# Optimization experiments

Hardware: AMD Instinct MI355X
Metric: run time of the kernel (lower is better)

Reference implementation:

```python
import jax, jax.numpy as jnp
import numpy as np

N = 100_000   # nodes
E = 1_600_000 # edges
F = 64        # in_feats
H = 64        # hid
EPS = 1e-5


def setup_inputs() -> dict:
    key = jax.random.key(0)
    ks = jax.random.split(key, 12)
    s = 1.0 / np.sqrt(F)
    inp = {
        "x":   jax.random.normal(ks[0], (N, F), jnp.float32),
        "src": jax.random.randint(ks[1], (E,), 0, N, jnp.int32),
        "dst": jax.random.randint(ks[2], (E,), 0, N, jnp.int32),
        # GraphConv 1: in_feats -> hid
        "W1": jax.random.uniform(ks[3], (F, H), jnp.float32, -s, s),
        "b1": jnp.zeros((H,), jnp.float32),
        "g1": jnp.ones((H,), jnp.float32),
        "be1": jnp.zeros((H,), jnp.float32),
        # GraphConv 2: hid -> hid
        "W2": jax.random.uniform(ks[4], (H, H), jnp.float32, -s, s),
        "b2": jnp.zeros((H,), jnp.float32),
        "g2": jnp.ones((H,), jnp.float32),
        "be2": jnp.zeros((H,), jnp.float32),
        # classifier hid -> 2
        "Wc": jax.random.uniform(ks[5], (H, 2), jnp.float32, -s, s),
        "bc": jnp.zeros((2,), jnp.float32),
    }
    return inp


def _graph_conv(x, src, dst, W, b):
    # DGL GraphConv, norm='both', allow_zero_in_degree=True:
    # h = D_in^{-1/2} A (D_out^{-1/2} x) W + b, degrees clamped to >= 1.
    n = x.shape[0]
    ones = jnp.ones(src.shape[0], x.dtype)
    deg_out = jnp.clip(jax.ops.segment_sum(ones, src, num_segments=n), 1.0)
    deg_in = jnp.clip(jax.ops.segment_sum(ones, dst, num_segments=n), 1.0)
    h = x * jax.lax.rsqrt(deg_out)[:, None]
    m = jax.ops.segment_sum(h[src], dst, num_segments=n)  # gather-scatter SpMM
    m = m * jax.lax.rsqrt(deg_in)[:, None]
    return m @ W + b


def _bn(h, g, be):
    # BatchNorm1d training-mode math over nodes (biased variance).
    mu = h.mean(axis=0)
    var = h.var(axis=0)
    return (h - mu) * jax.lax.rsqrt(var + EPS) * g + be


def reference(x, src, dst, W1, b1, g1, be1, W2, b2, g2, be2, Wc, bc):
    h = jax.nn.relu(_bn(_graph_conv(x, src, dst, W1, b1), g1, be1))
    # dropout is identity in eval mode
    h = jax.nn.relu(_bn(_graph_conv(h, src, dst, W2, b2), g2, be2))
    hg = h.mean(axis=0, keepdims=True)  # [1, H] graph readout
    return hg @ Wc + bc                 # [1, 2]
```

## Files before the change

kernel.cpp:

```cpp
#include <hip/hip_runtime.h>
#include <hip/hip_fp16.h>

#define FDIM 64
#define EPS 1e-5f
#define NBUCK 1024
#define LOWB 7
#define LOWMASK 127
#define RB 256
#define RT 1024
#define GRP 16
#define NSLOT 8

__global__ void k_hist(const int* __restrict__ src, const int* __restrict__ dst,
                       int* __restrict__ histS, int* __restrict__ histD, int E, int chunk) {
    __shared__ int hs[NBUCK], hd[NBUCK];
    int tid = threadIdx.x;
    hs[tid] = 0; hd[tid] = 0;
    __syncthreads();
    int b = blockIdx.x;
    int beg = b * chunk;
    int end = min(E, beg + chunk);
    int i = beg + tid * 4;
    for (; i + 3 < end; i += RT * 4) {
        int4 s = *(const int4*)(src + i);
        int4 d = *(const int4*)(dst + i);
        atomicAdd(&hs[s.x >> LOWB], 1); atomicAdd(&hd[d.x >> LOWB], 1);
        atomicAdd(&hs[s.y >> LOWB], 1); atomicAdd(&hd[d.y >> LOWB], 1);
        atomicAdd(&hs[s.z >> LOWB], 1); atomicAdd(&hd[d.z >> LOWB], 1);
        atomicAdd(&hs[s.w >> LOWB], 1); atomicAdd(&hd[d.w >> LOWB], 1);
    }
    if (i < end) {
        for (int j = i; j < end && j < i + 4; ++j) {
            atomicAdd(&hs[src[j] >> LOWB], 1);
            atomicAdd(&hd[dst[j] >> LOWB], 1);
        }
    }
    __syncthreads();
    histS[b * NBUCK + tid] = hs[tid];
    histD[b * NBUCK + tid] = hd[tid];
}

__global__ void k_scanA(const int* __restrict__ histS, const int* __restrict__ histD,
                        int* __restrict__ psumS, int* __restrict__ psumD) {
    int bid = blockIdx.x;
    int m = bid >> 6;
    int g = (bid >> 2) & (RB / GRP - 1);
    int c = bid & 3;
    const int* hist = m ? histD : histS;
    int* psum = m ? psumD : psumS;
    int k = c * 256 + threadIdx.x;
    int s = 0;
#pragma unroll
    for (int r = 0; r < GRP; ++r)
        s += hist[(g * GRP + r) * NBUCK + k];
    psum[g * NBUCK + k] = s;
}

__global__ void k_scanB(const int* __restrict__ psumS, int* __restrict__ baseS,
                        int* __restrict__ grpbaseS,
                        const int* __restrict__ psumD, int* __restrict__ baseD,
                        int* __restrict__ grpbaseD) {
    const int* psum = blockIdx.x ? psumD : psumS;
    int* base    = blockIdx.x ? baseD : baseS;
    int* grpbase = blockIdx.x ? grpbaseD : grpbaseS;
    __shared__ int s[NBUCK];
    int k = threadIdx.x;
    int ge[RB / GRP];
    int run = 0;
#pragma unroll
    for (int g = 0; g < RB / GRP; ++g) { ge[g] = run; run += psum[g * NBUCK + k]; }
    s[k] = run;
    __syncthreads();
    for (int off = 1; off < NBUCK; off <<= 1) {
        int t = (k >= off) ? s[k - off] : 0;
        __syncthreads();
        s[k] += t;
        __syncthreads();
    }
    int excl = (k > 0) ? s[k - 1] : 0;
    base[k] = excl;
    if (k == NBUCK - 1) base[NBUCK] = s[NBUCK - 1];
#pragma unroll
    for (int g = 0; g < RB / GRP; ++g)
        grpbase[g * NBUCK + k] = excl + ge[g];
}

__global__ void k_bucket(const int* __restrict__ src, const int* __restrict__ dst,
                         const int* __restrict__ histS, const int* __restrict__ histD,
                         const int* __restrict__ grpbaseS, const int* __restrict__ grpbaseD,
                         unsigned char* __restrict__ tmpS, int* __restrict__ tmpD,
                         int E, int chunk) {
    __shared__ int curS[NBUCK], curD[NBUCK];
    int tid = threadIdx.x;
    int b = blockIdx.x;
    int g = b / GRP;
    int rs = 0, rd = 0;
    for (int r = g * GRP; r < b; ++r) {
        rs += histS[r * NBUCK + tid];
        rd += histD[r * NBUCK + tid];
    }
    curS[tid] = grpbaseS[g * NBUCK + tid] + rs;
    curD[tid] = grpbaseD[g * NBUCK + tid] + rd;
    __syncthreads();
    int beg = b * chunk;
    int end = min(E, beg + chunk);
    int i = beg + tid * 4;
    for (; i + 3 < end; i += RT * 4) {
        int4 s = *(const int4*)(src + i);
        int4 d = *(const int4*)(dst + i);
        int p;
        p = atomicAdd(&curS[s.x >> LOWB], 1); tmpS[p] = (unsigned char)(s.x & LOWMASK);
        p = atomicAdd(&curS[s.y >> LOWB], 1); tmpS[p] = (unsigned char)(s.y & LOWMASK);
        p = atomicAdd(&curS[s.z >> LOWB], 1); tmpS[p] = (unsigned char)(s.z & LOWMASK);
        p = atomicAdd(&curS[s.w >> LOWB], 1); tmpS[p] = (unsigned char)(s.w & LOWMASK);
        p = atomicAdd(&curD[d.x >> LOWB], 1); tmpD[p] = (s.x << LOWB) | (d.x & LOWMASK);
        p = atomicAdd(&curD[d.y >> LOWB], 1); tmpD[p] = (s.y << LOWB) | (d.y & LOWMASK);
        p = atomicAdd(&curD[d.z >> LOWB], 1); tmpD[p] = (s.z << LOWB) | (d.z & LOWMASK);
        p = atomicAdd(&curD[d.w >> LOWB], 1); tmpD[p] = (s.w << LOWB) | (d.w & LOWMASK);
    }
    if (i < end) {
        for (int j = i; j < end && j < i + 4; ++j) {
            int sv = src[j], dv = dst[j];
            int p = atomicAdd(&curS[sv >> LOWB], 1);
            tmpS[p] = (unsigned char)(sv & LOWMASK);
            p = atomicAdd(&curD[dv >> LOWB], 1);
            tmpD[p] = (sv << LOWB) | (dv & LOWMASK);
        }
    }
}

__global__ void k_fine(const int* __restrict__ tmpD, const int* __restrict__ baseD,
                       int* __restrict__ csr_src, int* __restrict__ rowptr,
                       const unsigned char* __restrict__ tmpS, const int* __restrict__ baseS,
                       int* __restrict__ degO, const float* __restrict__ x,
                       __half* __restrict__ bufA, int N, int nbuck) {
    __shared__ int hist[128];
    __shared__ int scanv[128];
    int tid = threadIdx.x;
    if (blockIdx.x < nbuck) {
        int b = blockIdx.x;
        int s0 = baseD[b];
        int s1 = baseD[b + 1];
        if (tid < 128) hist[tid] = 0;
        __syncthreads();
        for (int i = s0 + tid; i < s1; i += 256)
            atomicAdd(&hist[tmpD[i] & LOWMASK], 1);
        __syncthreads();
        int mine = (tid < 128) ? hist[tid] : 0;
        if (tid < 128) scanv[tid] = mine;
        __syncthreads();
        for (int off = 1; off < 128; off <<= 1) {
            int t = (tid < 128 && tid >= off) ? scanv[tid - off] : 0;
            __syncthreads();
            if (tid < 128) scanv[tid] += t;
            __syncthreads();
        }
        if (tid < 128) {
            int excl = scanv[tid] - mine;
            int d = (b << LOWB) + tid;
            if (d <= N) rowptr[d] = s0 + excl;
            hist[tid] = excl;
        }
        __syncthreads();
        for (int i = s0 + tid; i < s1; i += 256) {
            int p = tmpD[i];
            int pos = atomicAdd(&hist[p & LOWMASK], 1);
            csr_src[s0 + pos] = p >> LOWB;
        }
    } else {
        int b = blockIdx.x - nbuck;
        int s0 = baseS[b];
        int s1 = baseS[b + 1];
        if (tid < 128) hist[tid] = 0;
        __syncthreads();
        for (int i = s0 + tid; i < s1; i += 256)
            atomicAdd(&hist[tmpS[i]], 1);
        __syncthreads();
        if (tid < 128) {
            int d = (b << LOWB) + tid;
            if (d < N) degO[d] = hist[tid];
        }
        int node = (b << LOWB) + (tid >> 1);
        if (node < N) {
            float rs = rsqrtf((float)max(hist[tid >> 1], 1));
            int part = tid & 1;
            const float4* xr = (const float4*)(x + (size_t)node * FDIM) + part * 8;
            float4* orow = (float4*)(bufA + (size_t)node * FDIM) + part * 4;
#pragma unroll
            for (int q = 0; q < 4; ++q) {
                float4 a = xr[2 * q];
                float4 c = xr[2 * q + 1];
                union { __half2 h[4]; float4 f; } u;
                u.h[0] = __floats2half2_rn(a.x * rs, a.y * rs);
                u.h[1] = __floats2half2_rn(a.z * rs, a.w * rs);
                u.h[2] = __floats2half2_rn(c.x * rs, c.y * rs);
                u.h[3] = __floats2half2_rn(c.z * rs, c.w * rs);
                orow[q] = u.f;
            }
        }
    }
}

__global__ void k_spmm8(const __half* __restrict__ hin, const int* __restrict__ rowptr,
                        const int* __restrict__ csr_src, __half* __restrict__ out, int N) {
    int wid = (blockIdx.x * blockDim.x + threadIdx.x) >> 6;
    int lane = threadIdx.x & 63;
    int g = lane >> 3;
    int sl = lane & 7;
    int row = wid * 8 + g;
    bool rv = row < N;
    int start = rv ? rowptr[row] : 0;
    int end   = rv ? rowptr[row + 1] : 0;
    int deg = end - start;
    int md = deg;
    md = max(md, __shfl_xor(md, 8));
    md = max(md, __shfl_xor(md, 16));
    md = max(md, __shfl_xor(md, 32));
    float acc[8] = {0.f, 0.f, 0.f, 0.f, 0.f, 0.f, 0.f, 0.f};
    for (int it = 0; it < md; it += 8) {
        int a = start + it + sl;
        int ca = (a < end) ? a : ((deg > 0) ? end - 1 : 0);
        int idxv = csr_src[ca];
#pragma unroll
        for (int j = 0; j < 8; ++j) {
            int bidx = __shfl(idxv, (g << 3) + j);
            if (it + j < deg) {
                const float4* gp = (const float4*)(hin + ((size_t)bidx << 6));
                union { float4 f; __half2 h[4]; } u;
                u.f = gp[sl];
                float2 p0 = __half22float2(u.h[0]);
                float2 p1 = __half22float2(u.h[1]);
                float2 p2 = __half22float2(u.h[2]);
                float2 p3 = __half22float2(u.h[3]);
                acc[0] += p0.x; acc[1] += p0.y;
                acc[2] += p1.x; acc[3] += p1.y;
                acc[4] += p2.x; acc[5] += p2.y;
                acc[6] += p3.x; acc[7] += p3.y;
            }
        }
    }
    if (rv) {
        float rs = rsqrtf(fmaxf((float)deg, 1.0f));
        union { float4 f; __half2 h[4]; } o;
        o.h[0] = __floats2half2_rn(acc[0] * rs, acc[1] * rs);
        o.h[1] = __floats2half2_rn(acc[2] * rs, acc[3] * rs);
        o.h[2] = __floats2half2_rn(acc[4] * rs, acc[5] * rs);
        o.h[3] = __floats2half2_rn(acc[6] * rs, acc[7] * rs);
        ((float4*)(out + ((size_t)row << 6)))[sl] = o.f;
    }
}

__global__ void k_gemm_reg(const __half* __restrict__ m, const float* __restrict__ W,
                           const float* __restrict__ b, __half* __restrict__ out, int N) {
    int n = blockIdx.x * blockDim.x + threadIdx.x;
    if (n >= N) return;
    const __half2* mrow = (const __half2*)(m + (size_t)n * FDIM);
    float acc[FDIM];
#pragma unroll
    for (int j = 0; j < FDIM; ++j) acc[j] = b[j];
    for (int k0 = 0; k0 < FDIM; k0 += 8) {
        float2 f0 = __half22float2(mrow[(k0 >> 1) + 0]);
        float2 f1 = __half22float2(mrow[(k0 >> 1) + 1]);
        float2 f2 = __half22float2(mrow[(k0 >> 1) + 2]);
        float2 f3 = __half22float2(mrow[(k0 >> 1) + 3]);
        float mreg[8] = {f0.x, f0.y, f1.x, f1.y, f2.x, f2.y, f3.x, f3.y};
#pragma unroll
        for (int k1 = 0; k1 < 8; ++k1) {
            const float* Wrow = W + (k0 + k1) * FDIM;
#pragma unroll
            for (int j = 0; j < FDIM; ++j)
                acc[j] = fmaf(mreg[k1], Wrow[j], acc[j]);
        }
    }
    float4* orow = (float4*)(out + (size_t)n * FDIM);
#pragma unroll
    for (int j = 0; j < FDIM; j += 8) {
        union { __half2 h[4]; float4 f; } u;
        u.h[0] = __floats2half2_rn(acc[j + 0], acc[j + 1]);
        u.h[1] = __floats2half2_rn(acc[j + 2], acc[j + 3]);
        u.h[2] = __floats2half2_rn(acc[j + 4], acc[j + 5]);
        u.h[3] = __floats2half2_rn(acc[j + 6], acc[j + 7]);
        orow[j >> 3] = u.f;
    }
}

__global__ void k_stats_fin(const __half* __restrict__ h, float* __restrict__ ssum,
                            float* __restrict__ ssq, const float* __restrict__ g,
                            float* __restrict__ mu, float* __restrict__ coef,
                            int* __restrict__ cnt, int N) {
    __shared__ float red[4][128];
    __shared__ int lastv;
    int tid = threadIdx.x;
    int sl = tid & 7;
    int nl = tid >> 3;
    float s[8] = {0.f,0.f,0.f,0.f,0.f,0.f,0.f,0.f};
    float q[8] = {0.f,0.f,0.f,0.f,0.f,0.f,0.f,0.f};
    int stride = gridDim.x * 32;
    for (int n = blockIdx.x * 32 + nl; n < N; n += stride) {
        union { float4 f; __half2 hh[4]; } u;
        u.f = ((const float4*)(h + ((size_t)n << 6)))[sl];
#pragma unroll
        for (int p = 0; p < 4; ++p) {
            float2 v = __half22float2(u.hh[p]);
            s[2*p]   += v.x; q[2*p]   += v.x * v.x;
            s[2*p+1] += v.y; q[2*p+1] += v.y * v.y;
        }
    }
#pragma unroll
    for (int off = 8; off < 64; off <<= 1) {
#pragma unroll
        for (int p = 0; p < 8; ++p) {
            s[p] += __shfl_xor(s[p], off);
            q[p] += __shfl_xor(q[p], off);
        }
    }
    int wv = tid >> 6, lane = tid & 63;
    if (lane < 8) {
#pragma unroll
        for (int p = 0; p < 8; ++p) {
            red[wv][lane * 8 + p] = s[p];
            red[wv][64 + lane * 8 + p] = q[p];
        }
    }
    __syncthreads();
    int slot = (blockIdx.x & (NSLOT - 1)) << 6;
    if (tid < 128) {
        float v = red[0][tid] + red[1][tid] + red[2][tid] + red[3][tid];
        if (tid < 64) atomicAdd(&ssum[slot + tid], v);
        else          atomicAdd(&ssq[slot + tid - 64], v);
    }
    __syncthreads();
    if (tid == 0)
        lastv = (__hip_atomic_fetch_add(cnt, 1, __ATOMIC_ACQ_REL,
                                        __HIP_MEMORY_SCOPE_AGENT) == (int)gridDim.x - 1);
    __syncthreads();
    if (lastv && tid < 64) {
        float sv = 0.f, qv = 0.f;
#pragma unroll
        for (int p = 0; p < NSLOT; ++p) {
            sv += __hip_atomic_load(&ssum[(p << 6) + tid], __ATOMIC_RELAXED,
                                    __HIP_MEMORY_SCOPE_AGENT);
            qv += __hip_atomic_load(&ssq[(p << 6) + tid], __ATOMIC_RELAXED,
                                    __HIP_MEMORY_SCOPE_AGENT);
        }
        float m = sv / (float)N;
        float var = qv / (float)N - m * m;
        mu[tid] = m;
        coef[tid] = rsqrtf(var + EPS) * g[tid];
    }
}

__global__ void k_bnrelu_scale(const float2* __restrict__ h, const float* __restrict__ mu,
                               const float* __restrict__ coef, const float* __restrict__ be,
                               const int* __restrict__ degO, float2* __restrict__ out, int n4) {
    int i = blockIdx.x * blockDim.x + threadIdx.x;
    if (i < n4) {
        int n = i >> 4;
        int j4 = (i & 15) << 2;
        float rs = rsqrtf((float)max(degO[n], 1));
        union { __half2 hh[2]; float2 f; } u;
        u.f = h[i];
        float2 v0 = __half22float2(u.hh[0]);
        float2 v1 = __half22float2(u.hh[1]);
        float r0 = fmaxf((v0.x - mu[j4 + 0]) * coef[j4 + 0] + be[j4 + 0], 0.f) * rs;
        float r1 = fmaxf((v0.y - mu[j4 + 1]) * coef[j4 + 1] + be[j4 + 1], 0.f) * rs;
        float r2 = fmaxf((v1.x - mu[j4 + 2]) * coef[j4 + 2] + be[j4 + 2], 0.f) * rs;
        float r3 = fmaxf((v1.y - mu[j4 + 3]) * coef[j4 + 3] + be[j4 + 3], 0.f) * rs;
        union { __half2 hh[2]; float2 f; } o;
        o.hh[0] = __floats2half2_rn(r0, r1);
        o.hh[1] = __floats2half2_rn(r2, r3);
        out[i] = o.f;
    }
}

__global__ void k_bnmean_fin(const __half* __restrict__ h, const float* __restrict__ mu,
                             const float* __restrict__ coef, const float* __restrict__ be,
                             float* __restrict__ hsum, const float* __restrict__ Wc,
                             const float* __restrict__ bc, float* __restrict__ out,
                             int* __restrict__ cnt, int N) {
    __shared__ float red[4][64];
    __shared__ float cls[128];
    __shared__ int lastv;
    int tid = threadIdx.x;
    int sl = tid & 7;
    int nl = tid >> 3;
    int j8 = sl * 8;
    float m_[8], c_[8], b_[8];
#pragma unroll
    for (int p = 0; p < 8; ++p) { m_[p] = mu[j8 + p]; c_[p] = coef[j8 + p]; b_[p] = be[j8 + p]; }
    float s[8] = {0.f,0.f,0.f,0.f,0.f,0.f,0.f,0.f};
    int stride = gridDim.x * 32;
    for (int n = blockIdx.x * 32 + nl; n < N; n += stride) {
        union { float4 f; __half2 hh[4]; } u;
        u.f = ((const float4*)(h + ((size_t)n << 6)))[sl];
#pragma unroll
        for (int p = 0; p < 4; ++p) {
            float2 v = __half22float2(u.hh[p]);
            s[2*p]   += fmaxf((v.x - m_[2*p])   * c_[2*p]   + b_[2*p],   0.f);
            s[2*p+1] += fmaxf((v.y - m_[2*p+1]) * c_[2*p+1] + b_[2*p+1], 0.f);
        }
    }
#pragma unroll
    for (int off = 8; off < 64; off <<= 1) {
#pragma unroll
        for (int p = 0; p < 8; ++p) s[p] += __shfl_xor(s[p], off);
    }
    int wv = tid >> 6, lane = tid & 63;
    if (lane < 8) {
#pragma unroll
        for (int p = 0; p < 8; ++p) red[wv][lane * 8 + p] = s[p];
    }
    __syncthreads();
    int slot = (blockIdx.x & (NSLOT - 1)) << 6;
    if (tid < 64)
        atomicAdd(&hsum[slot + tid], red[0][tid] + red[1][tid] + red[2][tid] + red[3][tid]);
    __syncthreads();
    if (tid == 0)
        lastv = (__hip_atomic_fetch_add(cnt, 1, __ATOMIC_ACQ_REL,
                                        __HIP_MEMORY_SCOPE_AGENT) == (int)gridDim.x - 1);
    __syncthreads();
    if (lastv) {
        if (tid < 64) {
            float hg = 0.f;
#pragma unroll
            for (int p = 0; p < NSLOT; ++p)
                hg += __hip_atomic_load(&hsum[(p << 6) + tid], __ATOMIC_RELAXED,
                                        __HIP_MEMORY_SCOPE_AGENT);
            hg /= (float)N;
            cls[tid]      = hg * Wc[tid * 2 + 0];
            cls[64 + tid] = hg * Wc[tid * 2 + 1];
        }
        __syncthreads();
        if (tid == 0) {
            float a = 0.f, bv = 0.f;
            for (int k = 0; k < 64; ++k) { a += cls[k]; bv += cls[64 + k]; }
            out[0] = a + bc[0];
            out[1] = bv + bc[1];
        }
    }
}

extern "C" void kernel_launch(void* const* d_in, const int* in_sizes, int n_in,
                              void* d_out, int out_size, void* d_ws, size_t ws_size,
                              hipStream_t stream) {
    const float* x   = (const float*)d_in[0];
    const int*   src = (const int*)d_in[1];
    const int*   dst = (const int*)d_in[2];
    const float* W1  = (const float*)d_in[3];
    const float* b1  = (const float*)d_in[4];
    const float* g1  = (const float*)d_in[5];
    const float* be1 = (const float*)d_in[6];
    const float* W2  = (const float*)d_in[7];
    const float* b2  = (const float*)d_in[8];
    const float* g2  = (const float*)d_in[9];
    const float* be2 = (const float*)d_in[10];
    const float* Wc  = (const float*)d_in[11];
    const float* bc  = (const float*)d_in[12];
    float* out = (float*)d_out;

    const int N = in_sizes[0] / FDIM;
    const int E = in_sizes[1];

    char* w = (char*)d_ws;
    __half* bufA   = (__half*)w;
    __half* bufB   = bufA + (size_t)N * FDIM;
    int*   csr_src = (int*)(bufB + (size_t)N * FDIM);
    int*   degO    = csr_src + E;
    int*   rowptr  = degO + N;
    int*   histS   = rowptr + N + 2;
    int*   histD   = histS + RB * NBUCK;
    int*   baseS   = histD + RB * NBUCK;
    int*   baseD   = baseS + NBUCK + 1;
    int*   psumS   = baseD + NBUCK + 1;
    int*   psumD   = psumS + (RB / GRP) * NBUCK;
    int*   grpbaseS= psumD + (RB / GRP) * NBUCK;
    int*   grpbaseD= grpbaseS + (RB / GRP) * NBUCK;
    float* stats   = (float*)(grpbaseD + (RB / GRP) * NBUCK);
    unsigned char* tmpS = (unsigned char*)(stats + 4096);
    int*           tmpD = (int*)bufB;

    float* sum1  = stats + 0;
    float* sq1   = stats + 512;
    float* sum2  = stats + 1024;
    float* sq2   = stats + 1536;
    float* hsum  = stats + 2048;
    float* mu1   = stats + 2560;
    float* coef1 = stats + 2624;
    float* mu2   = stats + 2688;
    float* coef2 = stats + 2752;
    int*   cnt1  = (int*)(stats + 2816);
    int*   cnt2  = (int*)(stats + 2817);
    int*   cnt3  = (int*)(stats + 2818);

    const int n4 = N * (FDIM / 4);
    const int spmm8_blocks = ((N + 7) / 8 + 3) / 4;
    const int nbuck_active = (N + LOWMASK) >> LOWB;
    const int chunk = ((E + RB - 1) / RB + 3) & ~3;

    hipMemsetAsync(stats, 0, 4096 * 4, stream);

    k_hist<<<RB, RT, 0, stream>>>(src, dst, histS, histD, E, chunk);
    k_scanA<<<2 * (RB / GRP) * 4, 256, 0, stream>>>(histS, histD, psumS, psumD);
    k_scanB<<<2, NBUCK, 0, stream>>>(psumS, baseS, grpbaseS, psumD, baseD, grpbaseD);
    k_bucket<<<RB, RT, 0, stream>>>(src, dst, histS, histD, grpbaseS, grpbaseD,
                                    tmpS, tmpD, E, chunk);
    k_fine<<<2 * nbuck_active, 256, 0, stream>>>(tmpD, baseD, csr_src, rowptr,
                                                 tmpS, baseS, degO, x, bufA, N, nbuck_active);

    k_spmm8<<<spmm8_blocks, 256, 0, stream>>>(bufA, rowptr, csr_src, bufB, N);
    k_gemm_reg<<<(N + 63) / 64, 64, 0, stream>>>(bufB, W1, b1, bufA, N);
    k_stats_fin<<<256, 256, 0, stream>>>(bufA, sum1, sq1, g1, mu1, coef1, cnt1, N);
    k_bnrelu_scale<<<(n4 + 255) / 256, 256, 0, stream>>>((const float2*)bufA, mu1, coef1, be1,
                                                         degO, (float2*)bufB, n4);
    k_spmm8<<<spmm8_blocks, 256, 0, stream>>>(bufB, rowptr, csr_src, bufA, N);
    k_gemm_reg<<<(N + 63) / 64, 64, 0, stream>>>(bufA, W2, b2, bufB, N);
    k_stats_fin<<<256, 256, 0, stream>>>(bufB, sum2, sq2, g2, mu2, coef2, cnt2, N);
    k_bnmean_fin<<<256, 256, 0, stream>>>(bufB, mu2, coef2, be2, hsum, Wc, bc, out, cnt3, N);
}
```

Before: 304.6 us.

## Fuse BN statistics into GEMM, merge scan kernels, drop stats memset

Computes the BatchNorm sum and sum-of-squares directly in the per-node GEMM epilogue using wave shuffles, so the separate stats kernel no longer re-reads the activations. The two scan kernels become one, in which the last-arriving block does the global prefix scan. The stats-buffer memset is folded into the histogram kernel. This cuts three launches and one full activation read per layer. In exchange the GEMM block grows from 64 to 256 threads, which adds register pressure, and the per-block reduction plus atomics now sit in the GEMM. Zeroing the stats from block 0 of the histogram kernel relies on that kernel finishing before the scan's counter is used.

```diff
diff --git a/kernel.cpp b/kernel.cpp
--- a/kernel.cpp
+++ b/kernel.cpp
@@ -12,12 +12,17 @@
 #define NSLOT 8
 
 __global__ void k_hist(const int* __restrict__ src, const int* __restrict__ dst,
-                       int* __restrict__ histS, int* __restrict__ histD, int E, int chunk) {
+                       int* __restrict__ histS, int* __restrict__ histD,
+                       float* __restrict__ statsZ, int E, int chunk) {
     __shared__ int hs[NBUCK], hd[NBUCK];
     int tid = threadIdx.x;
     hs[tid] = 0; hd[tid] = 0;
-    __syncthreads();
     int b = blockIdx.x;
+    if (b == 0) {
+#pragma unroll
+        for (int i = 0; i < 4; ++i) statsZ[i * RT + tid] = 0.f;
+    }
+    __syncthreads();
     int beg = b * chunk;
     int end = min(E, beg + chunk);
     int i = beg + tid * 4;
@@ -40,49 +45,57 @@
     histD[b * NBUCK + tid] = hd[tid];
 }
 
-__global__ void k_scanA(const int* __restrict__ histS, const int* __restrict__ histD,
-                        int* __restrict__ psumS, int* __restrict__ psumD) {
-    int bid = blockIdx.x;
-    int m = bid >> 6;
-    int g = (bid >> 2) & (RB / GRP - 1);
-    int c = bid & 3;
+__global__ void k_scanAB(const int* __restrict__ histS, const int* __restrict__ histD,
+                         int* __restrict__ psumS, int* __restrict__ psumD,
+                         int* __restrict__ baseS, int* __restrict__ grpbaseS,
+                         int* __restrict__ baseD, int* __restrict__ grpbaseD,
+                         int* __restrict__ cnt) {
+    __shared__ int sh[NBUCK];
+    __shared__ int lastv;
+    int tid = threadIdx.x;
+    int b = blockIdx.x;
+    int m = b >> 4, g = b & 15;
     const int* hist = m ? histD : histS;
     int* psum = m ? psumD : psumS;
-    int k = c * 256 + threadIdx.x;
     int s = 0;
 #pragma unroll
     for (int r = 0; r < GRP; ++r)
-        s += hist[(g * GRP + r) * NBUCK + k];
-    psum[g * NBUCK + k] = s;
-}
-
-__global__ void k_scanB(const int* __restrict__ psumS, int* __restrict__ baseS,
-                        int* __restrict__ grpbaseS,
-                        const int* __restrict__ psumD, int* __restrict__ baseD,
-                        int* __restrict__ grpbaseD) {
-    const int* psum = blockIdx.x ? psumD : psumS;
-    int* base    = blockIdx.x ? baseD : baseS;
-    int* grpbase = blockIdx.x ? grpbaseD : grpbaseS;
-    __shared__ int s[NBUCK];
-    int k = threadIdx.x;
-    int ge[RB / GRP];
-    int run = 0;
-#pragma unroll
-    for (int g = 0; g < RB / GRP; ++g) { ge[g] = run; run += psum[g * NBUCK + k]; }
-    s[k] = run;
-    __syncthreads();
-    for (int off = 1; off < NBUCK; off <<= 1) {
-        int t = (k >= off) ? s[k - off] : 0;
-        __syncthreads();
-        s[k] += t;
-        __syncthreads();
-    }
-    int excl = (k > 0) ? s[k - 1] : 0;
-    base[k] = excl;
-    if (k == NBUCK - 1) base[NBUCK] = s[NBUCK - 1];
-#pragma unroll
-    for (int g = 0; g < RB / GRP; ++g)
-        grpbase[g * NBUCK + k] = excl + ge[g];
+        s += hist[(g * GRP + r) * NBUCK + tid];
+    __hip_atomic_store(&psum[g * NBUCK + tid], s, __ATOMIC_RELEASE, __HIP_MEMORY_SCOPE_AGENT);
+    __syncthreads();
+    if (tid == 0)
+        lastv = (__hip_atomic_fetch_add(cnt, 1, __ATOMIC_ACQ_REL,
+                                        __HIP_MEMORY_SCOPE_AGENT) == (int)gridDim.x - 1);
+    __syncthreads();
+    if (!lastv) return;
+    for (int mm = 0; mm < 2; ++mm) {
+        const int* ps = mm ? psumD : psumS;
+        int* base    = mm ? baseD : baseS;
+        int* grpbase = mm ? grpbaseD : grpbaseS;
+        int ge[RB / GRP];
+        int run = 0;
+#pragma unroll
+        for (int gg = 0; gg < RB / GRP; ++gg) {
+            ge[gg] = run;
+            run += __hip_atomic_load(&ps[gg * NBUCK + tid], __ATOMIC_ACQUIRE,
+                                     __HIP_MEMORY_SCOPE_AGENT);
+        }
+        sh[tid] = run;
+        __syncthreads();
+        for (int off = 1; off < NBUCK; off <<= 1) {
+            int t = (tid >= off) ? sh[tid - off] : 0;
+            __syncthreads();
+            sh[tid] += t;
+            __syncthreads();
+        }
+        int excl = (tid > 0) ? sh[tid - 1] : 0;
+        base[tid] = excl;
+        if (tid == NBUCK - 1) base[NBUCK] = sh[NBUCK - 1];
+#pragma unroll
+        for (int gg = 0; gg < RB / GRP; ++gg)
+            grpbase[gg * NBUCK + tid] = excl + ge[gg];
+        __syncthreads();
+    }
 }
 
 __global__ void k_bucket(const int* __restrict__ src, const int* __restrict__ dst,
@@ -250,11 +263,17 @@
     }
 }
 
-__global__ void k_gemm_reg(const __half* __restrict__ m, const float* __restrict__ W,
-                           const float* __restrict__ b, __half* __restrict__ out, int N) {
-    int n = blockIdx.x * blockDim.x + threadIdx.x;
-    if (n >= N) return;
-    const __half2* mrow = (const __half2*)(m + (size_t)n * FDIM);
+__global__ void k_gemm_stats(const __half* __restrict__ m, const float* __restrict__ W,
+                             const float* __restrict__ b, __half* __restrict__ out,
+                             float* __restrict__ ssum, float* __restrict__ ssq,
+                             const float* __restrict__ g, float* __restrict__ mu,
+                             float* __restrict__ coef, int* __restrict__ cnt, int N) {
+    __shared__ float sred[4][128];
+    __shared__ int lastv;
+    int tid = threadIdx.x;
+    int n = blockIdx.x * blockDim.x + tid;
+    bool valid = n < N;
+    const __half2* mrow = (const __half2*)(m + ((size_t)(valid ? n : 0) << 6));
     float acc[FDIM];
 #pragma unroll
     for (int j = 0; j < FDIM; ++j) acc[j] = b[j];
@@ -272,60 +291,60 @@
                 acc[j] = fmaf(mreg[k1], Wrow[j], acc[j]);
         }
     }
-    float4* orow = (float4*)(out + (size_t)n * FDIM);
-#pragma unroll
-    for (int j = 0; j < FDIM; j += 8) {
-        union { __half2 h[4]; float4 f; } u;
-        u.h[0] = __floats2half2_rn(acc[j + 0], acc[j + 1]);
-        u.h[1] = __floats2half2_rn(acc[j + 2], acc[j + 3]);
-        u.h[2] = __floats2half2_rn(acc[j + 4], acc[j + 5]);
-        u.h[3] = __floats2half2_rn(acc[j + 6], acc[j + 7]);
-        orow[j >> 3] = u.f;
-    }
-}
-
-__global__ void k_stats_fin(const __half* __restrict__ h, float* __restrict__ ssum,
-                            float* __restrict__ ssq, const float* __restrict__ g,
-                            float* __restrict__ mu, float* __restrict__ coef,
-                            int* __restrict__ cnt, int N) {
-    __shared__ float red[4][128];
-    __shared__ int lastv;
-    int tid = threadIdx.x;
-    int sl = tid & 7;
-    int nl = tid >> 3;
-    float s[8] = {0.f,0.f,0.f,0.f,0.f,0.f,0.f,0.f};
-    float q[8] = {0.f,0.f,0.f,0.f,0.f,0.f,0.f,0.f};
-    int stride = gridDim.x * 32;
-    for (int n = blockIdx.x * 32 + nl; n < N; n += stride) {
-        union { float4 f; __half2 hh[4]; } u;
-        u.f = ((const float4*)(h + ((size_t)n << 6)))[sl];
-#pragma unroll
-        for (int p = 0; p < 4; ++p) {
-            float2 v = __half22float2(u.hh[p]);
-            s[2*p]   += v.x; q[2*p]   += v.x * v.x;
-            s[2*p+1] += v.y; q[2*p+1] += v.y * v.y;
-        }
-    }
-#pragma unroll
-    for (int off = 8; off < 64; off <<= 1) {
-#pragma unroll
-        for (int p = 0; p < 8; ++p) {
-            s[p] += __shfl_xor(s[p], off);
-            q[p] += __shfl_xor(q[p], off);
-        }
-    }
-    int wv = tid >> 6, lane = tid & 63;
-    if (lane < 8) {
-#pragma unroll
-        for (int p = 0; p < 8; ++p) {
-            red[wv][lane * 8 + p] = s[p];
-            red[wv][64 + lane * 8 + p] = q[p];
+    if (valid) {
+        float4* orow = (float4*)(out + ((size_t)n << 6));
+#pragma unroll
+        for (int j = 0; j < FDIM; j += 8) {
+            union { __half2 h[4]; float4 f; } u;
+            u.h[0] = __floats2half2_rn(acc[j + 0], acc[j + 1]);
+            u.h[1] = __floats2half2_rn(acc[j + 2], acc[j + 3]);
+            u.h[2] = __floats2half2_rn(acc[j + 4], acc[j + 5]);
+            u.h[3] = __floats2half2_rn(acc[j + 6], acc[j + 7]);
+            orow[j >> 3] = u.f;
+        }
+    }
+    int lane = tid & 63, wv = tid >> 6;
+    for (int c0 = 0; c0 < FDIM; c0 += 16) {
+        float cs[16], cq[16];
+#pragma unroll
+        for (int i = 0; i < 16; ++i) {
+            float v = valid ? acc[c0 + i] : 0.f;
+            cs[i] = v; cq[i] = v * v;
+        }
+#pragma unroll
+        for (int mm = 32; mm >= 16; mm >>= 1) {
+#pragma unroll
+            for (int i = 0; i < 16; ++i) {
+                cs[i] += __shfl_xor(cs[i], mm);
+                cq[i] += __shfl_xor(cq[i], mm);
+            }
+        }
+        int half = 8;
+#pragma unroll
+        for (int mm = 8; mm >= 1; mm >>= 1) {
+            bool up = (lane & mm) != 0;
+#pragma unroll
+            for (int i = 0; i < 8; ++i) {
+                if (i < half) {
+                    float ssnd = up ? cs[i] : cs[i + half];
+                    float qsnd = up ? cq[i] : cq[i + half];
+                    float srcv = __shfl_xor(ssnd, mm);
+                    float qrcv = __shfl_xor(qsnd, mm);
+                    cs[i] = (up ? cs[i + half] : cs[i]) + srcv;
+                    cq[i] = (up ? cq[i + half] : cq[i]) + qrcv;
+                }
+            }
+            half >>= 1;
+        }
+        if (lane < 16) {
+            sred[wv][c0 + lane] = cs[0];
+            sred[wv][64 + c0 + lane] = cq[0];
         }
     }
     __syncthreads();
     int slot = (blockIdx.x & (NSLOT - 1)) << 6;
     if (tid < 128) {
-        float v = red[0][tid] + red[1][tid] + red[2][tid] + red[3][tid];
+        float v = sred[0][tid] + sred[1][tid] + sred[2][tid] + sred[3][tid];
         if (tid < 64) atomicAdd(&ssum[slot + tid], v);
         else          atomicAdd(&ssq[slot + tid - 64], v);
     }
@@ -343,9 +362,9 @@
             qv += __hip_atomic_load(&ssq[(p << 6) + tid], __ATOMIC_RELAXED,
                                     __HIP_MEMORY_SCOPE_AGENT);
         }
-        float m = sv / (float)N;
-        float var = qv / (float)N - m * m;
-        mu[tid] = m;
+        float mv = sv / (float)N;
+        float var = qv / (float)N - mv * mv;
+        mu[tid] = mv;
         coef[tid] = rsqrtf(var + EPS) * g[tid];
     }
 }
@@ -491,29 +510,29 @@
     int*   cnt1  = (int*)(stats + 2816);
     int*   cnt2  = (int*)(stats + 2817);
     int*   cnt3  = (int*)(stats + 2818);
+    int*   cnt4  = (int*)(stats + 2819);
 
     const int n4 = N * (FDIM / 4);
     const int spmm8_blocks = ((N + 7) / 8 + 3) / 4;
     const int nbuck_active = (N + LOWMASK) >> LOWB;
     const int chunk = ((E + RB - 1) / RB + 3) & ~3;
-
-    hipMemsetAsync(stats, 0, 4096 * 4, stream);
-
-    k_hist<<<RB, RT, 0, stream>>>(src, dst, histS, histD, E, chunk);
-    k_scanA<<<2 * (RB / GRP) * 4, 256, 0, stream>>>(histS, histD, psumS, psumD);
-    k_scanB<<<2, NBUCK, 0, stream>>>(psumS, baseS, grpbaseS, psumD, baseD, grpbaseD);
+    const int gemm_blocks = (N + 255) / 256;
+
+    k_hist<<<RB, RT, 0, stream>>>(src, dst, histS, histD, stats, E, chunk);
+    k_scanAB<<<2 * (RB / GRP), RT, 0, stream>>>(histS, histD, psumS, psumD,
+                                                baseS, grpbaseS, baseD, grpbaseD, cnt4);
     k_bucket<<<RB, RT, 0, stream>>>(src, dst, histS, histD, grpbaseS, grpbaseD,
                                     tmpS, tmpD, E, chunk);
     k_fine<<<2 * nbuck_active, 256, 0, stream>>>(tmpD, baseD, csr_src, rowptr,
                                                  tmpS, baseS, degO, x, bufA, N, nbuck_active);
 
     k_spmm8<<<spmm8_blocks, 256, 0, stream>>>(bufA, rowptr, csr_src, bufB, N);
-    k_gemm_reg<<<(N + 63) / 64, 64, 0, stream>>>(bufB, W1, b1, bufA, N);
-    k_stats_fin<<<256, 256, 0, stream>>>(bufA, sum1, sq1, g1, mu1, coef1, cnt1, N);
+    k_gemm_stats<<<gemm_blocks, 256, 0, stream>>>(bufB, W1, b1, bufA, sum1, sq1,
+                                                  g1, mu1, coef1, cnt1, N);
     k_bnrelu_scale<<<(n4 + 255) / 256, 256, 0, stream>>>((const float2*)bufA, mu1, coef1, be1,
                                                          degO, (float2*)bufB, n4);
     k_spmm8<<<spmm8_blocks, 256, 0, stream>>>(bufB, rowptr, csr_src, bufA, N);
-    k_gemm_reg<<<(N + 63) / 64, 64, 0, stream>>>(bufA, W2, b2, bufB, N);
-    k_stats_fin<<<256, 256, 0, stream>>>(bufB, sum2, sq2, g2, mu2, coef2, cnt2, N);
+    k_gemm_stats<<<gemm_blocks, 256, 0, stream>>>(bufA, W2, b2, bufB, sum2, sq2,
+                                                  g2, mu2, coef2, cnt2, N);
     k_bnmean_fin<<<256, 256, 0, stream>>>(bufB, mu2, coef2, be2, hsum, Wc, bc, out, cnt3, N);
 }
```

Measured after the change: 431.5 us. +41.7%, slower.
